# Performance work log

Measured on AMD Instinct MI355X. Metric: run time of the kernel, lower is better.

## Reference

```python
import jax, jax.numpy as jnp
import numpy as np

NUM_CLUSTERS = 8
NUM_ITERS = 3
SIM_TEMP = 10.0
EPS = 1e-12  # F.normalize default eps


def _l2norm(x):
    n = jnp.linalg.norm(x, axis=-1, keepdims=True)
    return x / jnp.maximum(n, EPS)


def setup_inputs() -> dict:
    key = jax.random.key(0)
    ks = jax.random.split(key, 5)
    B, P, C = 8, 16384, 256
    F_p = jax.random.normal(ks[0], (B, P, C), dtype=jnp.float32)
    scale = 1.0 / np.sqrt(C)
    proj_w = jax.random.normal(ks[1], (C, C), dtype=jnp.float32) * scale
    proj_b = jax.random.normal(ks[2], (C,), dtype=jnp.float32) * scale
    refine_w = jax.random.normal(ks[3], (C, C), dtype=jnp.float32) * scale
    refine_b = jax.random.normal(ks[4], (C,), dtype=jnp.float32) * scale
    return {"F_p": F_p, "proj_w": proj_w, "proj_b": proj_b,
            "refine_w": refine_w, "refine_b": refine_b}


def reference(F_p, proj_w, proj_b, refine_w, refine_b):
    B, P, C = F_p.shape
    c = min(NUM_CLUSTERS, P)
    nodes = F_p @ proj_w.T + proj_b  # (B, P, C)
    # initial centers: evenly spaced node indices (torch.linspace(...).long())
    idx = jnp.asarray(np.linspace(0, P - 1, c).astype(np.int64))
    centers = nodes[:, idx, :]  # (B, c, C)
    nodes_norm = _l2norm(nodes)
    for _ in range(NUM_ITERS):
        sim = jnp.einsum('bpc,bkc->bpk', nodes_norm, _l2norm(centers))
        assignments = jnp.argmax(sim, axis=-1)  # (B, P)
        onehot = jax.nn.one_hot(assignments, c, dtype=nodes.dtype)  # (B, P, c)
        counts = jnp.maximum(onehot.sum(axis=1), 1.0)  # (B, c), clamp(min=1)
        # masked mean per cluster == segment mean via one-hot contraction
        centers = jnp.einsum('bpk,bpc->bkc', onehot, nodes) / counts[..., None]
    sim = jnp.einsum('bpc,bkc->bpk', nodes_norm, _l2norm(centers))
    weights = jax.nn.softmax(sim * SIM_TEMP, axis=-1)  # (B, P, c)
    clustered = jnp.einsum('bpk,bkc->bpc', weights, centers)
    return (clustered + F_p) @ refine_w.T + refine_b
```

## Files before the change

kernel.cpp:

```cpp
#include <hip/hip_runtime.h>
#include <hip/hip_bf16.h>
#include <cmath>

#define BB 8
#define PP 16384
#define CC 256
#define NCLUS 8
#define BPROWS (BB*PP)

typedef unsigned int uint;
typedef unsigned short ushort;
typedef __bf16 bf16x8 __attribute__((ext_vector_type(8)));
typedef float f32x16 __attribute__((ext_vector_type(16)));

__device__ __forceinline__ ushort f2bf(float x){ __hip_bfloat16 h = __float2bfloat16(x); return *(ushort*)&h; }
__device__ __forceinline__ uint pk2(float a, float b){ return (uint)f2bf(a) | ((uint)f2bf(b) << 16); }

__global__ __launch_bounds__(256) void wcvt(const float* __restrict__ Wp,
    const float* __restrict__ Wr, ushort* __restrict__ Wpb, ushort* __restrict__ Wrb) {
  int i = blockIdx.x*256 + threadIdx.x;
  float4 a = *(const float4*)(Wp + (size_t)i*4);
  float4 b = *(const float4*)(Wr + (size_t)i*4);
  *(uint2*)(Wpb + (size_t)i*4) = make_uint2(pk2(a.x,a.y), pk2(a.z,a.w));
  *(uint2*)(Wrb + (size_t)i*4) = make_uint2(pk2(b.x,b.y), pk2(b.z,b.w));
}

__device__ __forceinline__ void sims_mfma(const ushort* __restrict__ nb_base,
    const ushort* __restrict__ cnb, int lane, float* s) {
  const int pcol = lane & 31;
  const int kb   = (lane >> 5) << 3;
  const ushort* arow = cnb + (size_t)(pcol & 7)*CC + kb;
  const ushort* brow = nb_base + (size_t)pcol*CC + kb;
  const bool azero = pcol >= 8;
  bf16x8 z;
  #pragma unroll
  for (int j = 0; j < 8; ++j) z[j] = (__bf16)0.0f;
  f32x16 acc;
  #pragma unroll
  for (int r = 0; r < 16; ++r) acc[r] = 0.0f;
  #pragma unroll
  for (int st = 0; st < 16; ++st) {
    bf16x8 af = *(const bf16x8*)(arow + st*16);
    if (azero) af = z;
    bf16x8 bg = *(const bf16x8*)(brow + st*16);
    acc = __builtin_amdgcn_mfma_f32_32x32x16_bf16(af, bg, acc, 0, 0, 0);
  }
  float sh[4];
  #pragma unroll
  for (int r = 0; r < 4; ++r) sh[r] = __shfl_xor(acc[r], 32);
  const bool hi = lane >= 32;
  #pragma unroll
  for (int r = 0; r < 4; ++r) {
    s[r]     = hi ? sh[r]  : acc[r];
    s[r + 4] = hi ? acc[r] : sh[r];
  }
}

template<bool PROJ>
__global__ __launch_bounds__(512) void gemm_bf16(const float* __restrict__ A,
    const ushort* __restrict__ Wb, const float* __restrict__ bias,
    void* __restrict__ Dv, float* __restrict__ rnorm,
    const float* __restrict__ CR,
    const ushort* __restrict__ nbf, const ushort* __restrict__ cnormbf) {
  __shared__ __align__(16) char AlB[128*64*2];
  __shared__ __align__(16) char WlB[256*64*2];
  __shared__ __align__(16) float shr8[128][8];
  const int t  = threadIdx.x;
  const int p0 = blockIdx.x * 128;
  const int lane = t & 63;
  const int w  = t >> 6;
  const int wr = w >> 2, wc = w & 3;

  int aoff[2]; size_t agb[2];
  #pragma unroll
  for (int i = 0; i < 2; ++i) {
    int S = i*512 + t, row = S >> 3, sc = S & 7;
    aoff[i] = row*128 + ((sc*16) ^ ((row & 7) << 4));
    agb[i]  = (size_t)(p0 + row)*CC + sc*8;
  }
  const ushort* wsrc[4]; char* wdst[4];
  #pragma unroll
  for (int i = 0; i < 4; ++i) {
    int S = i*512 + t, row = S >> 3, sc = S & 7;
    wsrc[i] = Wb + (size_t)row*CC + ((sc ^ (row & 7)) << 3);
    wdst[i] = WlB + (size_t)S*16;
  }
  const int arow = (wr << 6) + (lane & 31);
  const int brow = (wc << 6) + (lane & 31);
  const int kb0  = (lane >> 5) << 4;

  uint4 ra[2];
  auto LOADA = [&](int ks) {
    #pragma unroll
    for (int i = 0; i < 2; ++i) {
      float4 v0 = *(const float4*)(A + agb[i] + ks*64);
      float4 v1 = *(const float4*)(A + agb[i] + ks*64 + 4);
      ra[i] = make_uint4(pk2(v0.x,v0.y), pk2(v0.z,v0.w), pk2(v1.x,v1.y), pk2(v1.z,v1.w));
    }
  };
  auto WRITEA = [&]() {
    #pragma unroll
    for (int i = 0; i < 2; ++i) *(uint4*)(AlB + aoff[i]) = ra[i];
  };
  auto STAGEW = [&](int ks) {
    #pragma unroll
    for (int i = 0; i < 4; ++i)
      __builtin_amdgcn_global_load_lds(
          (const __attribute__((address_space(1))) uint*)(wsrc[i] + ks*64),
          (__attribute__((address_space(3))) uint*)wdst[i], 16, 0, 0);
  };

  f32x16 acc[2][2];
  #pragma unroll
  for (int fm = 0; fm < 2; ++fm)
    #pragma unroll
    for (int fn = 0; fn < 2; ++fn)
      #pragma unroll
      for (int r = 0; r < 16; ++r) acc[fm][fn][r] = 0.0f;

  LOADA(0); STAGEW(0);
  if constexpr (!PROJ) {
    if (w < 4) {
      const size_t p0w = (size_t)p0 + w*32;
      float s[8];
      sims_mfma(nbf + p0w*CC, cnormbf + (size_t)(blockIdx.x >> 7)*NCLUS*CC, lane, s);
      const int pcol = lane & 31;
      const float rn10 = rnorm[p0w + pcol] * 10.0f;
      float m = -1e30f;
      #pragma unroll
      for (int k = 0; k < 8; ++k) { s[k] *= rn10; m = fmaxf(m, s[k]); }
      float wgt[8], sw = 0.0f;
      #pragma unroll
      for (int k = 0; k < 8; ++k) { wgt[k] = __expf(s[k] - m); sw += wgt[k]; }
      const float inv = 1.0f / sw;
      if (lane < 32) {
        float* wp = &shr8[w*32 + pcol][0];
        *(float4*)(wp)     = make_float4(wgt[0]*inv, wgt[1]*inv, wgt[2]*inv, wgt[3]*inv);
        *(float4*)(wp + 4) = make_float4(wgt[4]*inv, wgt[5]*inv, wgt[6]*inv, wgt[7]*inv);
      }
    }
  }
  WRITEA();
  __syncthreads();

  #pragma unroll
  for (int ks = 0; ks < 4; ++ks) {
    if (ks < 3) LOADA(ks + 1);
    bf16x8 af[2][4], bg[2][4];
    #pragma unroll
    for (int fm = 0; fm < 2; ++fm)
      #pragma unroll
      for (int kq = 0; kq < 4; ++kq) {
        int row = arow + (fm << 5);
        int off = row*128 + (((kq << 5) + kb0) ^ ((row & 7) << 4));
        af[fm][kq] = *(const bf16x8*)(AlB + off);
      }
    #pragma unroll
    for (int fn = 0; fn < 2; ++fn)
      #pragma unroll
      for (int kq = 0; kq < 4; ++kq) {
        int row = brow + (fn << 5);
        int off = row*128 + (((kq << 5) + kb0) ^ ((row & 7) << 4));
        bg[fn][kq] = *(const bf16x8*)(WlB + off);
      }
    #pragma unroll
    for (int kq = 0; kq < 4; ++kq)
      #pragma unroll
      for (int fm = 0; fm < 2; ++fm)
        #pragma unroll
        for (int fn = 0; fn < 2; ++fn)
          acc[fm][fn] = __builtin_amdgcn_mfma_f32_32x32x16_bf16(
              af[fm][kq], bg[fn][kq], acc[fm][fn], 0, 0, 0);
    if (ks < 3) {
      __syncthreads();
      STAGEW(ks + 1);
      WRITEA();
      __syncthreads();
    }
  }

  const int colb = (wc << 6) + (lane & 31);
  const float b0 = bias[colb], b1 = bias[colb + 32];
  float cr0[8], cr1[8];
  if constexpr (!PROJ) {
    const float* crb = CR + (size_t)(blockIdx.x >> 7)*NCLUS*CC;
    #pragma unroll
    for (int k = 0; k < 8; ++k) { cr0[k] = crb[k*CC + colb]; cr1[k] = crb[k*CC + colb + 32]; }
  }
  #pragma unroll
  for (int fm = 0; fm < 2; ++fm) {
    float rs[16];
    #pragma unroll
    for (int r = 0; r < 16; ++r) {
      int rowin = (r & 3) + ((r >> 2) << 3) + ((lane >> 5) << 2);
      int r128  = (wr << 6) + (fm << 5) + rowin;
      size_t grow = (size_t)(p0 + r128);
      float v0 = acc[fm][0][r] + b0;
      float v1 = acc[fm][1][r] + b1;
      if constexpr (PROJ) {
        ushort* D = (ushort*)Dv;
        D[grow*CC + colb]      = f2bf(v0);
        D[grow*CC + colb + 32] = f2bf(v1);
        rs[r] = v0*v0 + v1*v1;
      } else {
        float4 ua = *(const float4*)&shr8[r128][0];
        float4 ub = *(const float4*)&shr8[r128][4];
        v0 += ua.x*cr0[0] + ua.y*cr0[1] + ua.z*cr0[2] + ua.w*cr0[3]
            + ub.x*cr0[4] + ub.y*cr0[5] + ub.z*cr0[6] + ub.w*cr0[7];
        v1 += ua.x*cr1[0] + ua.y*cr1[1] + ua.z*cr1[2] + ua.w*cr1[3]
            + ub.x*cr1[4] + ub.y*cr1[5] + ub.z*cr1[6] + ub.w*cr1[7];
        float* D = (float*)Dv;
        D[grow*CC + colb]      = v0;
        D[grow*CC + colb + 32] = v1;
      }
    }
    if constexpr (PROJ) {
      #pragma unroll
      for (int m = 1; m < 32; m <<= 1)
        #pragma unroll
        for (int r = 0; r < 16; ++r) rs[r] += __shfl_xor(rs[r], m);
      if ((lane & 31) == 0) {
        #pragma unroll
        for (int r = 0; r < 16; ++r) {
          int rowin = (r & 3) + ((r >> 2) << 3) + ((lane >> 5) << 2);
          shr8[(wr << 6) + (fm << 5) + rowin][wc] = rs[r];
        }
      }
    }
  }
  if constexpr (PROJ) {
    __syncthreads();
    if (t < 128) {
      float s = shr8[t][0] + shr8[t][1] + shr8[t][2] + shr8[t][3];
      rnorm[p0 + t] = 1.0f / fmaxf(sqrtf(s), 1e-12f);
    }
  }
}

__global__ __launch_bounds__(256) void centers_init(const ushort* __restrict__ nbf,
    ushort* __restrict__ cnormbf, float* __restrict__ accs, float* __restrict__ counts) {
  const int idxs[8] = {0, 2340, 4680, 7021, 9361, 11702, 14042, 16383};
  const int row = blockIdx.x;
  const int b = row >> 3, k = row & 7;
  const int t = threadIdx.x;
  float c = __uint_as_float(((uint)nbf[((size_t)b*PP + idxs[k])*CC + t]) << 16);
  float s2 = c*c;
  #pragma unroll
  for (int o = 32; o; o >>= 1) s2 += __shfl_xor(s2, o);
  __shared__ float ps[4];
  if ((t & 63) == 0) ps[t >> 6] = s2;
  __syncthreads();
  float tot = ps[0] + ps[1] + ps[2] + ps[3];
  cnormbf[(size_t)row*CC + t] = f2bf(c * (1.0f / fmaxf(sqrtf(tot), 1e-12f)));
  #pragma unroll
  for (int s = 0; s < 8; ++s) accs[((size_t)s*64 + row)*CC + t] = 0.0f;
  if (t == 0) counts[row] = 0.0f;
}

template<bool DO_CR>
__global__ __launch_bounds__(256) void centers_finalize(float* __restrict__ accs,
    float* __restrict__ counts, ushort* __restrict__ cnormbf,
    const float* __restrict__ Wr, float* __restrict__ CR) {
  __shared__ float cenL[CC];
  const int row = blockIdx.x;
  const int t = threadIdx.x;
  float v = 0.0f;
  #pragma unroll
  for (int s = 0; s < 8; ++s) {
    v += accs[((size_t)s*64 + row)*CC + t];
    accs[((size_t)s*64 + row)*CC + t] = 0.0f;
  }
  float cnt = fmaxf(counts[row], 1.0f);
  float c = v / cnt;
  if constexpr (DO_CR) cenL[t] = c;
  float s2 = c*c;
  #pragma unroll
  for (int o = 32; o; o >>= 1) s2 += __shfl_xor(s2, o);
  __shared__ float ps[4];
  if ((t & 63) == 0) ps[t >> 6] = s2;
  __syncthreads();
  float tot = ps[0] + ps[1] + ps[2] + ps[3];
  cnormbf[(size_t)row*CC + t] = f2bf(c * (1.0f / fmaxf(sqrtf(tot), 1e-12f)));
  if (t == 0) counts[row] = 0.0f;
  if constexpr (DO_CR) {
    float a = 0.0f;
    const float* wrow = Wr + (size_t)t*CC;
    #pragma unroll 4
    for (int j = 0; j < CC; j += 4) {
      float4 wv = *(const float4*)(wrow + j);
      float4 cv = *(const float4*)&cenL[j];
      a += cv.x*wv.x + cv.y*wv.y + cv.z*wv.z + cv.w*wv.w;
    }
    CR[(size_t)row*CC + t] = a;
  }
}

__global__ __launch_bounds__(256) void assign_mfma(const ushort* __restrict__ nbf,
    const ushort* __restrict__ cnormbf, float* __restrict__ accs, float* __restrict__ counts) {
  __shared__ int assignL[128];
  __shared__ int cntL[NCLUS];
  const int t = threadIdx.x;
  const int wave = t >> 6, lane = t & 63;
  const int b = blockIdx.x >> 7;
  if (t < NCLUS) cntL[t] = 0;
  __syncthreads();
  const size_t p0w = (size_t)blockIdx.x*128 + wave*32;
  float s[8];
  sims_mfma(nbf + p0w*CC, cnormbf + (size_t)b*NCLUS*CC, lane, s);
  if (lane < 32) {
    int best = 0; float bs = s[0];
    #pragma unroll
    for (int k = 1; k < 8; ++k) if (s[k] > bs) { bs = s[k]; best = k; }
    assignL[wave*32 + lane] = best;
    atomicAdd(&cntL[best], 1);
  }
  __syncthreads();
  float a[8] = {0,0,0,0,0,0,0,0};
  const ushort* base = nbf + (size_t)blockIdx.x*128*CC;
  #pragma unroll 4
  for (int i = 0; i < 128; ++i) {
    int asg = __builtin_amdgcn_readfirstlane(assignL[i]);
    float v = __uint_as_float(((uint)base[(size_t)i*CC + t]) << 16);
    if      (asg == 0) a[0] += v;
    else if (asg == 1) a[1] += v;
    else if (asg == 2) a[2] += v;
    else if (asg == 3) a[3] += v;
    else if (asg == 4) a[4] += v;
    else if (asg == 5) a[5] += v;
    else if (asg == 6) a[6] += v;
    else               a[7] += v;
  }
  const int slot = blockIdx.x & 7;
  float* dst = accs + ((size_t)slot*BB + b)*NCLUS*CC;
  #pragma unroll
  for (int k = 0; k < 8; ++k) atomicAdd(&dst[k*CC + t], a[k]);
  if (t < NCLUS) atomicAdd(&counts[b*NCLUS + t], (float)cntL[t]);
}

extern "C" void kernel_launch(void* const* d_in, const int* in_sizes, int n_in,
                              void* d_out, int out_size, void* d_ws, size_t ws_size,
                              hipStream_t stream) {
  const float* F_p      = (const float*)d_in[0];
  const float* proj_w   = (const float*)d_in[1];
  const float* proj_b   = (const float*)d_in[2];
  const float* refine_w = (const float*)d_in[3];
  const float* refine_b = (const float*)d_in[4];
  float* out = (float*)d_out;

  char* ws = (char*)d_ws;
  ushort* nbf    = (ushort*)ws;
  float*  rnorm  = (float*)(ws + (size_t)BPROWS*CC*2);
  float*  accs   = rnorm + BPROWS;
  float*  counts = accs + 8*BB*NCLUS*CC;
  float*  CR     = counts + 64;
  ushort* cnormbf= (ushort*)(CR + BB*NCLUS*CC);
  ushort* Wpb    = cnormbf + BB*NCLUS*CC;
  ushort* Wrb    = Wpb + CC*CC;

  wcvt<<<64, 256, 0, stream>>>(proj_w, refine_w, Wpb, Wrb);
  gemm_bf16<true><<<1024, 512, 0, stream>>>(F_p, Wpb, proj_b, nbf, rnorm,
                                            nullptr, nullptr, nullptr);
  centers_init<<<64, 256, 0, stream>>>(nbf, cnormbf, accs, counts);
  for (int it = 0; it < 3; ++it) {
    assign_mfma<<<1024, 256, 0, stream>>>(nbf, cnormbf, accs, counts);
    if (it < 2) centers_finalize<false><<<64, 256, 0, stream>>>(accs, counts, cnormbf, nullptr, nullptr);
    else        centers_finalize<true ><<<64, 256, 0, stream>>>(accs, counts, cnormbf, refine_w, CR);
  }
  gemm_bf16<false><<<1024, 512, 0, stream>>>(F_p, Wrb, refine_b, out, rnorm,
                                             CR, nbf, cnormbf);
}
```

Before: 276.6 us.

## Split GEMM output columns across two blocks and accumulate row norms atomically

Both bf16 GEMM kernels now launch a 2D grid so that each block computes a 128x128 output tile instead of 128x256. This halves the per-block weight LDS tile and the accumulator registers, with the aim of raising occupancy and parallelism. Because a row's squared norm is now split across two blocks, partial sums are combined with atomicAdd into a buffer that the weight-conversion kernel zeroes, and the consumer computes the reciprocal norm itself. In exchange, each block pair reads the fp32 input rows twice, and the refine pass repeats the similarity and softmax prologue in both column blocks.

```diff
diff --git a/kernel.cpp b/kernel.cpp
--- a/kernel.cpp
+++ b/kernel.cpp
@@ -17,12 +17,16 @@
 __device__ __forceinline__ uint pk2(float a, float b){ return (uint)f2bf(a) | ((uint)f2bf(b) << 16); }
 
 __global__ __launch_bounds__(256) void wcvt(const float* __restrict__ Wp,
-    const float* __restrict__ Wr, ushort* __restrict__ Wpb, ushort* __restrict__ Wrb) {
+    const float* __restrict__ Wr, ushort* __restrict__ Wpb, ushort* __restrict__ Wrb,
+    float* __restrict__ rsum) {
   int i = blockIdx.x*256 + threadIdx.x;
   float4 a = *(const float4*)(Wp + (size_t)i*4);
   float4 b = *(const float4*)(Wr + (size_t)i*4);
   *(uint2*)(Wpb + (size_t)i*4) = make_uint2(pk2(a.x,a.y), pk2(a.z,a.w));
   *(uint2*)(Wrb + (size_t)i*4) = make_uint2(pk2(b.x,b.y), pk2(b.z,b.w));
+  float4 z = make_float4(0.f,0.f,0.f,0.f);
+  *(float4*)(rsum + (size_t)i*8)     = z;
+  *(float4*)(rsum + (size_t)i*8 + 4) = z;
 }
 
 __device__ __forceinline__ void sims_mfma(const ushort* __restrict__ nb_base,
@@ -59,17 +63,18 @@
 template<bool PROJ>
 __global__ __launch_bounds__(512) void gemm_bf16(const float* __restrict__ A,
     const ushort* __restrict__ Wb, const float* __restrict__ bias,
-    void* __restrict__ Dv, float* __restrict__ rnorm,
+    void* __restrict__ Dv, float* __restrict__ rsum,
     const float* __restrict__ CR,
     const ushort* __restrict__ nbf, const ushort* __restrict__ cnormbf) {
   __shared__ __align__(16) char AlB[128*64*2];
-  __shared__ __align__(16) char WlB[256*64*2];
+  __shared__ __align__(16) char WlB[128*64*2];
   __shared__ __align__(16) float shr8[128][8];
   const int t  = threadIdx.x;
   const int p0 = blockIdx.x * 128;
+  const int n0 = blockIdx.y * 128;
   const int lane = t & 63;
   const int w  = t >> 6;
-  const int wr = w >> 2, wc = w & 3;
+  const int wr = w >> 1, wc = w & 1;
 
   int aoff[2]; size_t agb[2];
   #pragma unroll
@@ -78,14 +83,14 @@
     aoff[i] = row*128 + ((sc*16) ^ ((row & 7) << 4));
     agb[i]  = (size_t)(p0 + row)*CC + sc*8;
   }
-  const ushort* wsrc[4]; char* wdst[4];
-  #pragma unroll
-  for (int i = 0; i < 4; ++i) {
+  const ushort* wsrc[2]; char* wdst[2];
+  #pragma unroll
+  for (int i = 0; i < 2; ++i) {
     int S = i*512 + t, row = S >> 3, sc = S & 7;
-    wsrc[i] = Wb + (size_t)row*CC + ((sc ^ (row & 7)) << 3);
+    wsrc[i] = Wb + (size_t)(n0 + row)*CC + ((sc ^ (row & 7)) << 3);
     wdst[i] = WlB + (size_t)S*16;
   }
-  const int arow = (wr << 6) + (lane & 31);
+  const int arow = (wr << 5) + (lane & 31);
   const int brow = (wc << 6) + (lane & 31);
   const int kb0  = (lane >> 5) << 4;
 
@@ -104,19 +109,17 @@
   };
   auto STAGEW = [&](int ks) {
     #pragma unroll
-    for (int i = 0; i < 4; ++i)
+    for (int i = 0; i < 2; ++i)
       __builtin_amdgcn_global_load_lds(
           (const __attribute__((address_space(1))) uint*)(wsrc[i] + ks*64),
           (__attribute__((address_space(3))) uint*)wdst[i], 16, 0, 0);
   };
 
-  f32x16 acc[2][2];
-  #pragma unroll
-  for (int fm = 0; fm < 2; ++fm)
-    #pragma unroll
-    for (int fn = 0; fn < 2; ++fn)
-      #pragma unroll
-      for (int r = 0; r < 16; ++r) acc[fm][fn][r] = 0.0f;
+  f32x16 acc[2];
+  #pragma unroll
+  for (int fn = 0; fn < 2; ++fn)
+    #pragma unroll
+    for (int r = 0; r < 16; ++r) acc[fn][r] = 0.0f;
 
   LOADA(0); STAGEW(0);
   if constexpr (!PROJ) {
@@ -125,7 +128,7 @@
       float s[8];
       sims_mfma(nbf + p0w*CC, cnormbf + (size_t)(blockIdx.x >> 7)*NCLUS*CC, lane, s);
       const int pcol = lane & 31;
-      const float rn10 = rnorm[p0w + pcol] * 10.0f;
+      const float rn10 = 10.0f / fmaxf(sqrtf(rsum[p0w + pcol]), 1e-12f);
       float m = -1e30f;
       #pragma unroll
       for (int k = 0; k < 8; ++k) { s[k] *= rn10; m = fmaxf(m, s[k]); }
@@ -146,15 +149,13 @@
   #pragma unroll
   for (int ks = 0; ks < 4; ++ks) {
     if (ks < 3) LOADA(ks + 1);
-    bf16x8 af[2][4], bg[2][4];
-    #pragma unroll
-    for (int fm = 0; fm < 2; ++fm)
-      #pragma unroll
-      for (int kq = 0; kq < 4; ++kq) {
-        int row = arow + (fm << 5);
-        int off = row*128 + (((kq << 5) + kb0) ^ ((row & 7) << 4));
-        af[fm][kq] = *(const bf16x8*)(AlB + off);
-      }
+    bf16x8 af[4], bg[2][4];
+    #pragma unroll
+    for (int kq = 0; kq < 4; ++kq) {
+      int row = arow;
+      int off = row*128 + (((kq << 5) + kb0) ^ ((row & 7) << 4));
+      af[kq] = *(const bf16x8*)(AlB + off);
+    }
     #pragma unroll
     for (int fn = 0; fn < 2; ++fn)
       #pragma unroll
@@ -166,11 +167,9 @@
     #pragma unroll
     for (int kq = 0; kq < 4; ++kq)
       #pragma unroll
-      for (int fm = 0; fm < 2; ++fm)
-        #pragma unroll
-        for (int fn = 0; fn < 2; ++fn)
-          acc[fm][fn] = __builtin_amdgcn_mfma_f32_32x32x16_bf16(
-              af[fm][kq], bg[fn][kq], acc[fm][fn], 0, 0, 0);
+      for (int fn = 0; fn < 2; ++fn)
+        acc[fn] = __builtin_amdgcn_mfma_f32_32x32x16_bf16(
+            af[kq], bg[fn][kq], acc[fn], 0, 0, 0);
     if (ks < 3) {
       __syncthreads();
       STAGEW(ks + 1);
@@ -179,7 +178,7 @@
     }
   }
 
-  const int colb = (wc << 6) + (lane & 31);
+  const int colb = n0 + (wc << 6) + (lane & 31);
   const float b0 = bias[colb], b1 = bias[colb + 32];
   float cr0[8], cr1[8];
   if constexpr (!PROJ) {
@@ -187,52 +186,47 @@
     #pragma unroll
     for (int k = 0; k < 8; ++k) { cr0[k] = crb[k*CC + colb]; cr1[k] = crb[k*CC + colb + 32]; }
   }
-  #pragma unroll
-  for (int fm = 0; fm < 2; ++fm) {
-    float rs[16];
-    #pragma unroll
-    for (int r = 0; r < 16; ++r) {
-      int rowin = (r & 3) + ((r >> 2) << 3) + ((lane >> 5) << 2);
-      int r128  = (wr << 6) + (fm << 5) + rowin;
-      size_t grow = (size_t)(p0 + r128);
-      float v0 = acc[fm][0][r] + b0;
-      float v1 = acc[fm][1][r] + b1;
-      if constexpr (PROJ) {
-        ushort* D = (ushort*)Dv;
-        D[grow*CC + colb]      = f2bf(v0);
-        D[grow*CC + colb + 32] = f2bf(v1);
-        rs[r] = v0*v0 + v1*v1;
-      } else {
-        float4 ua = *(const float4*)&shr8[r128][0];
-        float4 ub = *(const float4*)&shr8[r128][4];
-        v0 += ua.x*cr0[0] + ua.y*cr0[1] + ua.z*cr0[2] + ua.w*cr0[3]
-            + ub.x*cr0[4] + ub.y*cr0[5] + ub.z*cr0[6] + ub.w*cr0[7];
-        v1 += ua.x*cr1[0] + ua.y*cr1[1] + ua.z*cr1[2] + ua.w*cr1[3]
-            + ub.x*cr1[4] + ub.y*cr1[5] + ub.z*cr1[6] + ub.w*cr1[7];
-        float* D = (float*)Dv;
-        D[grow*CC + colb]      = v0;
-        D[grow*CC + colb + 32] = v1;
+  float rs[16];
+  #pragma unroll
+  for (int r = 0; r < 16; ++r) {
+    int rowin = (r & 3) + ((r >> 2) << 3) + ((lane >> 5) << 2);
+    int r128  = (wr << 5) + rowin;
+    size_t grow = (size_t)(p0 + r128);
+    float v0 = acc[0][r] + b0;
+    float v1 = acc[1][r] + b1;
+    if constexpr (PROJ) {
+      ushort* D = (ushort*)Dv;
+      D[grow*CC + colb]      = f2bf(v0);
+      D[grow*CC + colb + 32] = f2bf(v1);
+      rs[r] = v0*v0 + v1*v1;
+    } else {
+      float4 ua = *(const float4*)&shr8[r128][0];
+      float4 ub = *(const float4*)&shr8[r128][4];
+      v0 += ua.x*cr0[0] + ua.y*cr0[1] + ua.z*cr0[2] + ua.w*cr0[3]
+          + ub.x*cr0[4] + ub.y*cr0[5] + ub.z*cr0[6] + ub.w*cr0[7];
+      v1 += ua.x*cr1[0] + ua.y*cr1[1] + ua.z*cr1[2] + ua.w*cr1[3]
+          + ub.x*cr1[4] + ub.y*cr1[5] + ub.z*cr1[6] + ub.w*cr1[7];
+      float* D = (float*)Dv;
+      D[grow*CC + colb]      = v0;
+      D[grow*CC + colb + 32] = v1;
+    }
+  }
+  if constexpr (PROJ) {
+    #pragma unroll
+    for (int m = 1; m < 32; m <<= 1)
+      #pragma unroll
+      for (int r = 0; r < 16; ++r) rs[r] += __shfl_xor(rs[r], m);
+    __syncthreads();
+    if ((lane & 31) == 0) {
+      #pragma unroll
+      for (int r = 0; r < 16; ++r) {
+        int rowin = (r & 3) + ((r >> 2) << 3) + ((lane >> 5) << 2);
+        shr8[(wr << 5) + rowin][wc] = rs[r];
       }
     }
-    if constexpr (PROJ) {
-      #pragma unroll
-      for (int m = 1; m < 32; m <<= 1)
-        #pragma unroll
-        for (int r = 0; r < 16; ++r) rs[r] += __shfl_xor(rs[r], m);
-      if ((lane & 31) == 0) {
-        #pragma unroll
-        for (int r = 0; r < 16; ++r) {
-          int rowin = (r & 3) + ((r >> 2) << 3) + ((lane >> 5) << 2);
-          shr8[(wr << 6) + (fm << 5) + rowin][wc] = rs[r];
-        }
-      }
-    }
-  }
-  if constexpr (PROJ) {
     __syncthreads();
     if (t < 128) {
-      float s = shr8[t][0] + shr8[t][1] + shr8[t][2] + shr8[t][3];
-      rnorm[p0 + t] = 1.0f / fmaxf(sqrtf(s), 1e-12f);
+      atomicAdd(&rsum[p0 + t], shr8[t][0] + shr8[t][1]);
     }
   }
 }
@@ -349,23 +343,23 @@
 
   char* ws = (char*)d_ws;
   ushort* nbf    = (ushort*)ws;
-  float*  rnorm  = (float*)(ws + (size_t)BPROWS*CC*2);
-  float*  accs   = rnorm + BPROWS;
+  float*  rsum   = (float*)(ws + (size_t)BPROWS*CC*2);
+  float*  accs   = rsum + BPROWS;
   float*  counts = accs + 8*BB*NCLUS*CC;
   float*  CR     = counts + 64;
   ushort* cnormbf= (ushort*)(CR + BB*NCLUS*CC);
   ushort* Wpb    = cnormbf + BB*NCLUS*CC;
   ushort* Wrb    = Wpb + CC*CC;
 
-  wcvt<<<64, 256, 0, stream>>>(proj_w, refine_w, Wpb, Wrb);
-  gemm_bf16<true><<<1024, 512, 0, stream>>>(F_p, Wpb, proj_b, nbf, rnorm,
-                                            nullptr, nullptr, nullptr);
+  wcvt<<<64, 256, 0, stream>>>(proj_w, refine_w, Wpb, Wrb, rsum);
+  gemm_bf16<true><<<dim3(1024, 2), 512, 0, stream>>>(F_p, Wpb, proj_b, nbf, rsum,
+                                                     nullptr, nullptr, nullptr);
   centers_init<<<64, 256, 0, stream>>>(nbf, cnormbf, accs, counts);
   for (int it = 0; it < 3; ++it) {
     assign_mfma<<<1024, 256, 0, stream>>>(nbf, cnormbf, accs, counts);
     if (it < 2) centers_finalize<false><<<64, 256, 0, stream>>>(accs, counts, cnormbf, nullptr, nullptr);
     else        centers_finalize<true ><<<64, 256, 0, stream>>>(accs, counts, cnormbf, refine_w, CR);
   }
-  gemm_bf16<false><<<1024, 512, 0, stream>>>(F_p, Wrb, refine_b, out, rnorm,
-                                             CR, nbf, cnormbf);
-}
+  gemm_bf16<false><<<dim3(1024, 2), 512, 0, stream>>>(F_p, Wrb, refine_b, out, rsum,
+                                                      CR, nbf, cnormbf);
+}
```

Result: slower. 304.7 us (+10.1%).
